# Optimization experiments

Measured on AMD Instinct MI355X. Metric: run time of the kernel, lower is better.

Reference implementation:

```python
import jax, jax.numpy as jnp
import numpy as np

N_NODES = 50000
N_EDGES = 800000
N_GRAPHS = 64
NEG_SLOPE = 0.2  # PyG GATConv default leaky_relu slope
EPS = 1e-16      # PyG softmax denominator epsilon


def gat_conv(x, W, a_src, a_dst, bias, src, dst, n_nodes):
    """PyG GATConv (heads=1, concat=True, self-loops already appended).
    x: [N, F_in], W: [F_in, H*F], a_src/a_dst: [H, F], bias: [H*F]."""
    H, F = a_src.shape
    h = (x @ W).reshape(-1, H, F)                      # [N, H, F]
    alpha_src = jnp.einsum('nhf,hf->nh', h, a_src)     # [N, H]
    alpha_dst = jnp.einsum('nhf,hf->nh', h, a_dst)     # [N, H]
    e = jax.nn.leaky_relu(alpha_src[src] + alpha_dst[dst], NEG_SLOPE)  # [E, H]
    # segment softmax over incoming edges of each destination node
    e_max = jax.ops.segment_max(e, dst, num_segments=n_nodes)          # [N, H]
    e_exp = jnp.exp(e - e_max[dst])
    denom = jax.ops.segment_sum(e_exp, dst, num_segments=n_nodes)      # [N, H]
    alpha = e_exp / (denom[dst] + EPS)                                 # [E, H]
    msg = alpha[:, :, None] * h[src]                                   # [E, H, F]
    out = jax.ops.segment_sum(msg, dst, num_segments=n_nodes)          # [N, H, F]
    return out.reshape(-1, H * F) + bias


def global_mean_pool(x, batch, n_graphs):
    s = jax.ops.segment_sum(x, batch, num_segments=n_graphs)
    cnt = jax.ops.segment_sum(jnp.ones((x.shape[0],), x.dtype), batch, num_segments=n_graphs)
    return s / jnp.maximum(cnt, 1.0)[:, None]


def setup_inputs() -> dict:
    key = jax.random.key(0)
    ks = jax.random.split(key, 10)
    d_in, d_h, d_out, L, H = 128, 128, 10, 3, 1
    x = jax.random.normal(ks[0], (N_NODES, d_in), dtype=jnp.float32)
    edge_index = jax.random.randint(ks[1], (2, N_EDGES), 0, N_NODES, dtype=jnp.int32)
    edge_attr = jax.random.normal(ks[2], (N_EDGES, 4), dtype=jnp.float32)
    batch = jnp.sort(jax.random.randint(ks[3], (N_NODES,), 0, N_GRAPHS, dtype=jnp.int32))
    s0 = 1.0 / np.sqrt(d_in)
    sh = 1.0 / np.sqrt(d_h)
    return {
        'x': x,
        'edge_index': edge_index,
        'edge_attr': edge_attr,
        'batch': batch,
        'W0': jax.random.normal(ks[4], (d_in, d_h), dtype=jnp.float32) * s0,
        'b0': jnp.zeros((d_h,), jnp.float32),
        'Wc': jax.random.normal(ks[5], (L, d_h, H * d_h), dtype=jnp.float32) * sh,
        'att_src': jax.random.normal(ks[6], (L, H, d_h), dtype=jnp.float32) * sh,
        'att_dst': jax.random.normal(ks[7], (L, H, d_h), dtype=jnp.float32) * sh,
        'bc': jnp.zeros((L, H * d_h), jnp.float32),
        'W1': jax.random.normal(ks[8], (d_h, d_out), dtype=jnp.float32) * sh,
        'b1': jnp.zeros((d_out,), jnp.float32),
    }


def reference(x, edge_index, edge_attr, batch, W0, b0, Wc, att_src, att_dst, bc, W1, b1):
    n = x.shape[0]
    # GATConv default add_self_loops=True
    loops = jnp.arange(n, dtype=edge_index.dtype)
    src = jnp.concatenate([edge_index[0], loops])
    dst = jnp.concatenate([edge_index[1], loops])
    # dropout p=0 / eval mode -> identity
    h = jax.nn.relu(x @ W0 + b0)
    for i in range(Wc.shape[0]):
        h = jax.nn.relu(gat_conv(h, Wc[i], att_src[i], att_dst[i], bc[i], src, dst, n))
    pooled = global_mean_pool(h, batch, N_GRAPHS)   # [B, d_h]
    return pooled @ W1 + b1                          # [B, d_out]
```

## Files before the change

kernel.cpp:

```cpp
#include <hip/hip_runtime.h>
#include <hip/hip_bf16.h>
#include <hip/hip_fp16.h>
#include <hip/hip_fp8.h>

#define NN 50000
#define NE 800000
#define NG 64
#define DH 128

#define SEG 64
#define GEMMB 512
#define GEMMW (GEMMB * 4)
#define CST 136
#define CSTB 136
#define SMEM_BYTES 17408
#define NPAIR (NN / 2)
#define NXCD 8
#define XNODES (NN / NXCD)
#define CHUNKE 4096
#define NCHUNK ((NE + CHUNKE - 1) / CHUNKE)
#define SCATB (NCHUNK * NXCD)
#define WTB 256
#define INITB ((NN + 255) / 256)
#define PREPB (SCATB + WTB + INITB)

#if defined(__has_builtin)
# if __has_builtin(__builtin_amdgcn_cvt_pk_f32_fp8) && __has_builtin(__builtin_amdgcn_cvt_pk_f32_fp8)
# endif
# if __has_builtin(__builtin_amdgcn_cvt_pk_f32_fp8) && __has_builtin(__builtin_amdgcn_cvt_pk_fp8_f32)
#  define HW_FP8 1
# endif
#endif

typedef __bf16 bfx8 __attribute__((ext_vector_type(8)));
typedef float  f32x4 __attribute__((ext_vector_type(4)));
typedef float  f32x8 __attribute__((ext_vector_type(8)));

__device__ __forceinline__ ushort f2b(float f) {
    unsigned b = __float_as_uint(f);
    b += 0x7fff + ((b >> 16) & 1);
    return (ushort)(b >> 16);
}
__device__ __forceinline__ float b2f(ushort s) {
    return __uint_as_float((unsigned)s << 16);
}
__device__ __forceinline__ unsigned pk2(float a, float b) {
    return (unsigned)f2b(a) | ((unsigned)f2b(b) << 16);
}

__device__ __forceinline__ unsigned f2fp8(float v) {
    v = fminf(fmaxf(v, -448.f), 448.f);
#ifdef HW_FP8
    return (unsigned)__builtin_amdgcn_cvt_pk_fp8_f32(v, v, 0, false) & 0xFFu;
#else
    __hip_fp8_e4m3 t(v);
    return (unsigned)*(const unsigned char*)&t;
#endif
}
__device__ __forceinline__ void fp8x4_up(unsigned u, float* o) {
#ifdef HW_FP8
    auto lo = __builtin_amdgcn_cvt_pk_f32_fp8((int)u, false);
    auto hi = __builtin_amdgcn_cvt_pk_f32_fp8((int)u, true);
    o[0] = lo[0]; o[1] = lo[1]; o[2] = hi[0]; o[3] = hi[1];
#else
    #pragma unroll
    for (int k = 0; k < 4; ++k) {
        unsigned char c = (u >> (8 * k)) & 0xFF;
        o[k] = float(*(const __hip_fp8_e4m3*)&c);
    }
#endif
}

__launch_bounds__(256)
__global__ void k_prep(const int* __restrict__ ei, int* __restrict__ cur,
                       ushort* __restrict__ csr,
                       const float* __restrict__ W0, const float* __restrict__ Wc,
                       ushort* __restrict__ Wt) {
    int t = threadIdx.x;
    unsigned bid = blockIdx.x;
    if (bid < SCATB) {
        int chunk = bid >> 3;
        int lo = (int)(bid & 7) * XNODES;
        int base = chunk * CHUNKE + t;
        #pragma unroll
        for (int jj = 0; jj < 16; jj += 4) {
            int dd[4], ee[4];
            #pragma unroll
            for (int q = 0; q < 4; ++q) {
                ee[q] = base + (jj + q) * 256;
                dd[q] = (ee[q] < NE) ? ei[NE + ee[q]] : -1;
            }
            #pragma unroll
            for (int q = 0; q < 4; ++q) {
                if ((unsigned)(dd[q] - lo) < (unsigned)XNODES) {
                    int s = ei[ee[q]];
                    int slot = atomicAdd(&cur[dd[q]], 1);
                    if (slot < SEG - 1)
                        csr[((size_t)dd[q] << 6) + 1 + slot] = (ushort)s;
                }
            }
        }
        return;
    }
    if (bid < SCATB + WTB) {
        int i = (bid - SCATB) * 256 + t;
        int m = i >> 14;
        int r = i & 16383;
        int k = r >> 7, n = r & 127;
        const float* src = (m == 0) ? W0 : (Wc + (size_t)(m - 1) * DH * DH);
        Wt[(size_t)m * DH * DH + n * DH + k] = f2b(src[r]);
        return;
    }
    int n = (bid - SCATB - WTB) * 256 + t;
    if (n < NN) csr[(size_t)n << 6] = (ushort)n;
}

template<bool AF32, bool DOTS, bool OUTFP8>
__device__ __forceinline__ void gemm_body(char* smem, int gblk,
        const void* __restrict__ Av, const ushort* __restrict__ Wt,
        const float* __restrict__ bias, void* __restrict__ C, int relu,
        const float* __restrict__ avs, const float* __restrict__ avd,
        float* __restrict__ asrc, float* __restrict__ adst) {
    const int NT = NN / 16;
    int tid = threadIdx.x;
    int lane = tid & 63;
    int mrow = lane & 15;
    int quad = lane >> 4;
    int wid = (gblk * 256 + tid) >> 6;

    bfx8 b[4][8];
    #pragma unroll
    for (int ks = 0; ks < 4; ++ks) {
        int k0 = ks * 32 + quad * 8;
        #pragma unroll
        for (int t = 0; t < 8; ++t)
            b[ks][t] = *(const bfx8*)(Wt + (size_t)(t * 16 + mrow) * DH + k0);
    }
    float av[8], dv[8];
    if (DOTS) {
        #pragma unroll
        for (int t = 0; t < 8; ++t) {
            av[t] = avs[t * 16 + mrow];
            dv[t] = avd[t * 16 + mrow];
        }
    }

    for (int tile = wid; tile < NT; tile += GEMMW) {
        int row0 = tile * 16;
        int arow = row0 + mrow;

        bfx8 a[4];
        if (AF32) {
            f32x8 af[4];
            #pragma unroll
            for (int ks = 0; ks < 4; ++ks)
                af[ks] = *(const f32x8*)((const float*)Av + (size_t)arow * DH + ks * 32 + quad * 8);
            #pragma unroll
            for (int ks = 0; ks < 4; ++ks) {
                union { ushort s[8]; bfx8 v; } u;
                #pragma unroll
                for (int j = 0; j < 8; ++j) u.s[j] = f2b(af[ks][j]);
                a[ks] = u.v;
            }
        } else {
            #pragma unroll
            for (int ks = 0; ks < 4; ++ks)
                a[ks] = *(const bfx8*)((const ushort*)Av + (size_t)arow * DH + ks * 32 + quad * 8);
        }

        f32x4 acc[8];
        #pragma unroll
        for (int t = 0; t < 8; ++t)
            #pragma unroll
            for (int r = 0; r < 4; ++r) acc[t][r] = 0.f;

        #pragma unroll
        for (int ks = 0; ks < 4; ++ks)
            #pragma unroll
            for (int t = 0; t < 8; ++t)
                acc[t] = __builtin_amdgcn_mfma_f32_16x16x32_bf16(a[ks], b[ks][t], acc[t], 0, 0, 0);

        if (OUTFP8) {
            uchar* my = (uchar*)smem + (tid >> 6) * 16 * CSTB;
            #pragma unroll
            for (int t = 0; t < 8; ++t) {
                int col = t * 16 + mrow;
                float bv = bias ? bias[col] : 0.f;
                #pragma unroll
                for (int r = 0; r < 4; ++r) {
                    float v = acc[t][r] + bv;
                    if (relu) v = fmaxf(v, 0.f);
                    my[(quad * 4 + r) * CSTB + col] = (uchar)f2fp8(v);
                }
            }
            #pragma unroll
            for (int i = 0; i < 4; ++i) {
                int idx = i * 64 + lane;
                int row = idx >> 4;
                int c8 = idx & 15;
                uint2 u = *(const uint2*)(my + row * CSTB + c8 * 8);
                *(uint2*)((uchar*)C + (size_t)(row0 + row) * DH + c8 * 8) = u;
            }
        } else {
            ushort* my = (ushort*)smem + (tid >> 6) * 16 * CST;
            #pragma unroll
            for (int t = 0; t < 8; ++t) {
                int col = t * 16 + mrow;
                float bv = bias ? bias[col] : 0.f;
                #pragma unroll
                for (int r = 0; r < 4; ++r) {
                    float v = acc[t][r] + bv;
                    if (relu) v = fmaxf(v, 0.f);
                    my[(quad * 4 + r) * CST + col] = f2b(v);
                }
            }
            #pragma unroll
            for (int i = 0; i < 4; ++i) {
                int idx = i * 64 + lane;
                int row = idx >> 4;
                int c16 = idx & 15;
                uint4 u = *(const uint4*)(my + row * CST + c16 * 8);
                *(uint4*)((ushort*)C + (size_t)(row0 + row) * DH + c16 * 8) = u;
            }
        }

        if (DOTS) {
            int orow = row0 + quad * 4;
            #pragma unroll
            for (int r = 0; r < 4; ++r) {
                float ps = 0.f, pd = 0.f;
                #pragma unroll
                for (int t = 0; t < 8; ++t) {
                    ps += acc[t][r] * av[t];
                    pd += acc[t][r] * dv[t];
                }
                #pragma unroll
                for (int off = 1; off < 16; off <<= 1) {
                    ps += __shfl_xor(ps, off);
                    pd += __shfl_xor(pd, off);
                }
                if (mrow == 0) {
                    asrc[orow + r] = ps;
                    adst[orow + r] = pd;
                }
            }
        }
    }
}

__launch_bounds__(256)
__global__ void k_gemm1(const float* __restrict__ x, const ushort* __restrict__ Wt,
                        const float* __restrict__ b0, ushort* __restrict__ hB) {
    __shared__ char smem[SMEM_BYTES];
    gemm_body<true, false, false>(smem, blockIdx.x, x, Wt, b0, hB, 1,
                                  nullptr, nullptr, nullptr, nullptr);
}

__launch_bounds__(256)
__global__ void k_gemmdots(const ushort* __restrict__ hB, const ushort* __restrict__ Wt,
                           uchar* __restrict__ hA,
                           const float* __restrict__ avs, const float* __restrict__ avd,
                           float* __restrict__ asrc, float* __restrict__ adst) {
    __shared__ char smem[SMEM_BYTES];
    gemm_body<false, true, true>(smem, blockIdx.x, hB, Wt, nullptr, hA, 0,
                                 avs, avd, asrc, adst);
}

__device__ __forceinline__ void aggr_one(int wid, int lane,
        const uchar* __restrict__ h8, const float* __restrict__ asrc,
        const float* __restrict__ adst, const int* __restrict__ cur,
        const ushort* __restrict__ csr,
        const float* __restrict__ bias, ushort* __restrict__ hout) {
    int start = wid << 6;
    int cnt = min(cur[wid] + 1, SEG);
    float ad = adst[wid];

    int s = csr[start + lane];
    float e = -1e30f;
    if (lane < cnt) {
        float t = asrc[s] + ad;
        e = fmaxf(t, 0.f) + 0.2f * fminf(t, 0.f);
    }
    float m = e;
    #pragma unroll
    for (int off = 32; off; off >>= 1) m = fmaxf(m, __shfl_xor(m, off));
    float w = (lane < cnt) ? __expf(e - m) : 0.f;
    float dsum = w;
    #pragma unroll
    for (int off = 32; off; off >>= 1) dsum += __shfl_xor(dsum, off);

    int g = lane >> 4, fidx = lane & 15;
    float acc[8];
    #pragma unroll
    for (int k = 0; k < 8; ++k) acc[k] = 0.f;

    int steps = (cnt + 3) >> 2;
    const uint2* hp = (const uint2*)h8;
    for (int j = 0; j < steps; ++j) {
        int e0 = j * 4 + g;
        float w0 = __shfl(w, e0);
        int   s0 = __shfl(s, e0);
        uint2 u0 = hp[(size_t)s0 * 16 + fidx];
        float v[8];
        fp8x4_up(u0.x, v); fp8x4_up(u0.y, v + 4);
        #pragma unroll
        for (int k = 0; k < 8; ++k) acc[k] += w0 * v[k];
    }
    #pragma unroll
    for (int k = 0; k < 8; ++k) {
        acc[k] += __shfl_xor(acc[k], 16);
        acc[k] += __shfl_xor(acc[k], 32);
    }
    if (g == 0) {
        float inv = 1.f / (dsum + 1e-16f);
        const float4* bp = (const float4*)bias;
        float4 b0 = bp[fidx * 2], b1 = bp[fidx * 2 + 1];
        uint4 o;
        o.x = pk2(fmaxf(acc[0] * inv + b0.x, 0.f), fmaxf(acc[1] * inv + b0.y, 0.f));
        o.y = pk2(fmaxf(acc[2] * inv + b0.z, 0.f), fmaxf(acc[3] * inv + b0.w, 0.f));
        o.z = pk2(fmaxf(acc[4] * inv + b1.x, 0.f), fmaxf(acc[5] * inv + b1.y, 0.f));
        o.w = pk2(fmaxf(acc[6] * inv + b1.z, 0.f), fmaxf(acc[7] * inv + b1.w, 0.f));
        ((uint4*)hout)[(size_t)wid * 16 + fidx] = o;
    }
}

__launch_bounds__(256)
__global__ void k_aggr(const uchar* __restrict__ h8, const float* __restrict__ asrc,
                       const float* __restrict__ adst, const int* __restrict__ cur,
                       const ushort* __restrict__ csr,
                       const float* __restrict__ bias, ushort* __restrict__ hout) {
    int pid = (blockIdx.x * blockDim.x + threadIdx.x) >> 6;
    int lane = threadIdx.x & 63;
    if (pid >= NPAIR) return;
    int half = lane >> 5, hl = lane & 31;
    int nd = pid * 2 + half;
    int start = nd << 6;

    int cnt = min(cur[nd] + 1, SEG);
    int cother = __shfl_xor(cnt, 32);
    if (max(cnt, cother) <= 32) {
        float ad = adst[nd];
        int s = csr[start + hl];
        float e = -1e30f;
        if (hl < cnt) {
            float t = asrc[s] + ad;
            e = fmaxf(t, 0.f) + 0.2f * fminf(t, 0.f);
        }
        float m = e;
        #pragma unroll
        for (int off = 16; off; off >>= 1) m = fmaxf(m, __shfl_xor(m, off));
        float w = (hl < cnt) ? __expf(e - m) : 0.f;
        float dsum = w;
        #pragma unroll
        for (int off = 16; off; off >>= 1) dsum += __shfl_xor(dsum, off);

        int g = hl >> 4, fidx = hl & 15;
        int lbase = half * 32;
        float acc[8];
        #pragma unroll
        for (int k = 0; k < 8; ++k) acc[k] = 0.f;

        int steps = (cnt + 1) >> 1;
        const uint2* hp = (const uint2*)h8;
        int j = 0;
        for (; j + 3 < steps; j += 4) {
            int   e0 = j * 2 + g,       e1 = e0 + 2, e2 = e0 + 4, e3 = e0 + 6;
            float w0 = __shfl(w, lbase + e0), w1 = __shfl(w, lbase + e1);
            float w2 = __shfl(w, lbase + e2), w3 = __shfl(w, lbase + e3);
            int   s0 = __shfl(s, lbase + e0), s1 = __shfl(s, lbase + e1);
            int   s2 = __shfl(s, lbase + e2), s3 = __shfl(s, lbase + e3);
            uint2 u0 = hp[(size_t)s0 * 16 + fidx];
            uint2 u1 = hp[(size_t)s1 * 16 + fidx];
            uint2 u2 = hp[(size_t)s2 * 16 + fidx];
            uint2 u3 = hp[(size_t)s3 * 16 + fidx];
            float v[8];
            fp8x4_up(u0.x, v); fp8x4_up(u0.y, v + 4);
            #pragma unroll
            for (int k = 0; k < 8; ++k) acc[k] += w0 * v[k];
            fp8x4_up(u1.x, v); fp8x4_up(u1.y, v + 4);
            #pragma unroll
            for (int k = 0; k < 8; ++k) acc[k] += w1 * v[k];
            fp8x4_up(u2.x, v); fp8x4_up(u2.y, v + 4);
            #pragma unroll
            for (int k = 0; k < 8; ++k) acc[k] += w2 * v[k];
            fp8x4_up(u3.x, v); fp8x4_up(u3.y, v + 4);
            #pragma unroll
            for (int k = 0; k < 8; ++k) acc[k] += w3 * v[k];
        }
        for (; j < steps; ++j) {
            int   e0 = j * 2 + g;
            float w0 = __shfl(w, lbase + e0);
            int   s0 = __shfl(s, lbase + e0);
            uint2 u0 = hp[(size_t)s0 * 16 + fidx];
            float v[8];
            fp8x4_up(u0.x, v); fp8x4_up(u0.y, v + 4);
            #pragma unroll
            for (int k = 0; k < 8; ++k) acc[k] += w0 * v[k];
        }
        #pragma unroll
        for (int k = 0; k < 8; ++k) acc[k] += __shfl_xor(acc[k], 16);
        if (g == 0) {
            float inv = 1.f / (dsum + 1e-16f);
            const float4* bp = (const float4*)bias;
            float4 b0 = bp[fidx * 2], b1 = bp[fidx * 2 + 1];
            uint4 o;
            o.x = pk2(fmaxf(acc[0] * inv + b0.x, 0.f), fmaxf(acc[1] * inv + b0.y, 0.f));
            o.y = pk2(fmaxf(acc[2] * inv + b0.z, 0.f), fmaxf(acc[3] * inv + b0.w, 0.f));
            o.z = pk2(fmaxf(acc[4] * inv + b1.x, 0.f), fmaxf(acc[5] * inv + b1.y, 0.f));
            o.w = pk2(fmaxf(acc[6] * inv + b1.z, 0.f), fmaxf(acc[7] * inv + b1.w, 0.f));
            ((uint4*)hout)[(size_t)nd * 16 + fidx] = o;
        }
        return;
    }

    aggr_one(pid * 2,     lane, h8, asrc, adst, cur, csr, bias, hout);
    aggr_one(pid * 2 + 1, lane, h8, asrc, adst, cur, csr, bias, hout);
}

__launch_bounds__(256)
__global__ void k_pool(const ushort* __restrict__ h, const int* __restrict__ batch,
                       float* __restrict__ gsum, int* __restrict__ gcnt) {
    int slot = threadIdx.x >> 7;
    int f = threadIdx.x & 127;
    int n0 = blockIdx.x * 64;
    int n1 = min(n0 + 64, NN);
    int first = n0 + slot;
    if (first >= n1) return;
    int g0 = batch[n0], g1 = batch[n1 - 1];
    if (g0 == g1) {
        float acc = 0.f;
        for (int nd = first; nd < n1; nd += 2)
            acc += b2f(h[(size_t)nd * DH + f]);
        atomicAdd(&gsum[g0 * DH + f], acc);
        if (f == 0 && slot == 0) atomicAdd(&gcnt[g0], n1 - n0);
        return;
    }
    float acc = 0.f; int run = 0;
    int gcur = batch[first];
    for (int nd = first; nd < n1; nd += 2) {
        int g = batch[nd];
        if (g != gcur) {
            atomicAdd(&gsum[gcur * DH + f], acc);
            if (f == 0) atomicAdd(&gcnt[gcur], run);
            acc = 0.f; run = 0; gcur = g;
        }
        acc += b2f(h[(size_t)nd * DH + f]);
        run += 1;
    }
    atomicAdd(&gsum[gcur * DH + f], acc);
    if (f == 0) atomicAdd(&gcnt[gcur], run);
}

__global__ void k_final(const float* __restrict__ gsum, const int* __restrict__ gcnt,
                        const float* __restrict__ W1, const float* __restrict__ b1,
                        float* __restrict__ out) {
    int t = threadIdx.x;
    if (t >= NG * 10) return;
    int g = t / 10, o = t % 10;
    float inv = 1.f / fmaxf((float)gcnt[g], 1.f);
    float acc = 0.f;
    for (int f = 0; f < DH; ++f) acc += gsum[g * DH + f] * W1[f * 10 + o];
    out[t] = acc * inv + b1[o];
}

extern "C" void kernel_launch(void* const* d_in, const int* in_sizes, int n_in,
                              void* d_out, int out_size, void* d_ws, size_t ws_size,
                              hipStream_t stream) {
    const float* x       = (const float*)d_in[0];
    const int*   ei      = (const int*)d_in[1];
    const int*   batch   = (const int*)d_in[3];
    const float* W0      = (const float*)d_in[4];
    const float* b0      = (const float*)d_in[5];
    const float* Wc      = (const float*)d_in[6];
    const float* att_src = (const float*)d_in[7];
    const float* att_dst = (const float*)d_in[8];
    const float* bc      = (const float*)d_in[9];
    const float* W1      = (const float*)d_in[10];
    const float* b1      = (const float*)d_in[11];
    float* out = (float*)d_out;

    char* ws = (char*)d_ws;
    size_t off = 0;
    auto alloc = [&](size_t bytes) {
        void* p = ws + off;
        off += (bytes + 255) & ~(size_t)255;
        return p;
    };
    uchar*    hA     = (uchar*)alloc((size_t)NN * DH);
    ushort*   hB     = (ushort*)alloc((size_t)NN * DH * 2);
    ushort*   Wt     = (ushort*)alloc((size_t)4 * DH * DH * 2);
    ushort*   csr    = (ushort*)alloc((size_t)NN * SEG * 2);
    int*      cur    = (int*)alloc((size_t)NN * 4);
    float*    asrc   = (float*)alloc(NN * 4);
    float*    adst   = (float*)alloc(NN * 4);
    float*    gsum   = (float*)alloc(NG * DH * 4);
    int*      gcnt   = (int*)alloc(NG * 4);

    hipMemsetAsync(csr, 0, (size_t)NN * SEG * 2 + (size_t)NN * 4, stream);
    hipMemsetAsync(gsum, 0, NG * DH * 4 + 256, stream);

    k_prep<<<PREPB, 256, 0, stream>>>(ei, cur, csr, W0, Wc, Wt);
    k_gemm1<<<GEMMB, 256, 0, stream>>>(x, Wt, b0, hB);

    for (int l = 0; l < 3; ++l) {
        k_gemmdots<<<GEMMB, 256, 0, stream>>>(hB, Wt + (size_t)(l + 1) * DH * DH, hA,
                                              att_src + l * DH, att_dst + l * DH,
                                              asrc, adst);
        k_aggr<<<(NPAIR + 3) / 4, 256, 0, stream>>>(hA, asrc, adst, cur, csr,
                                                    bc + l * DH, hB);
    }

    k_pool<<<(NN + 63) / 64, 256, 0, stream>>>(hB, batch, gsum, gcnt);
    k_final<<<1, NG * 10, 0, stream>>>(gsum, gcnt, W1, b1, out);
}
```

Baseline: 302.0 us.

## Fuse pooling and final linear into one per-graph kernel, shrink memsets

Replaces the atomic-based mean-pool kernel and the separate final linear kernel with a single kernel that launches one block per graph. Each block binary-searches the sorted batch array for its node range, sums rows with 16-byte vector loads, reduces through shared memory and applies W1. The large memset of the CSR buffer is dropped, and CSR reads are masked to valid lanes so stale entries are never used. This removes two memsets' worth of traffic, the atomics and one launch, but leaves only 64 blocks for the pooling read, which may limit parallelism.

```diff
diff --git a/kernel.cpp b/kernel.cpp
--- a/kernel.cpp
+++ b/kernel.cpp
@@ -25,8 +25,6 @@
 #define PREPB (SCATB + WTB + INITB)
 
 #if defined(__has_builtin)
-# if __has_builtin(__builtin_amdgcn_cvt_pk_f32_fp8) && __has_builtin(__builtin_amdgcn_cvt_pk_f32_fp8)
-# endif
 # if __has_builtin(__builtin_amdgcn_cvt_pk_f32_fp8) && __has_builtin(__builtin_amdgcn_cvt_pk_fp8_f32)
 #  define HW_FP8 1
 # endif
@@ -35,6 +33,7 @@
 typedef __bf16 bfx8 __attribute__((ext_vector_type(8)));
 typedef float  f32x4 __attribute__((ext_vector_type(4)));
 typedef float  f32x8 __attribute__((ext_vector_type(8)));
+typedef short  s16x8 __attribute__((ext_vector_type(8)));
 
 __device__ __forceinline__ ushort f2b(float f) {
     unsigned b = __float_as_uint(f);
@@ -275,7 +274,7 @@
     int cnt = min(cur[wid] + 1, SEG);
     float ad = adst[wid];
 
-    int s = csr[start + lane];
+    int s = (lane < cnt) ? (int)csr[start + lane] : 0;
     float e = -1e30f;
     if (lane < cnt) {
         float t = asrc[s] + ad;
@@ -340,7 +339,7 @@
     int cother = __shfl_xor(cnt, 32);
     if (max(cnt, cother) <= 32) {
         float ad = adst[nd];
-        int s = csr[start + hl];
+        int s = (hl < cnt) ? (int)csr[start + hl] : 0;
         float e = -1e30f;
         if (hl < cnt) {
             float t = asrc[s] + ad;
@@ -418,49 +417,48 @@
 }
 
 __launch_bounds__(256)
-__global__ void k_pool(const ushort* __restrict__ h, const int* __restrict__ batch,
-                       float* __restrict__ gsum, int* __restrict__ gcnt) {
-    int slot = threadIdx.x >> 7;
-    int f = threadIdx.x & 127;
-    int n0 = blockIdx.x * 64;
-    int n1 = min(n0 + 64, NN);
-    int first = n0 + slot;
-    if (first >= n1) return;
-    int g0 = batch[n0], g1 = batch[n1 - 1];
-    if (g0 == g1) {
-        float acc = 0.f;
-        for (int nd = first; nd < n1; nd += 2)
-            acc += b2f(h[(size_t)nd * DH + f]);
-        atomicAdd(&gsum[g0 * DH + f], acc);
-        if (f == 0 && slot == 0) atomicAdd(&gcnt[g0], n1 - n0);
-        return;
-    }
-    float acc = 0.f; int run = 0;
-    int gcur = batch[first];
-    for (int nd = first; nd < n1; nd += 2) {
-        int g = batch[nd];
-        if (g != gcur) {
-            atomicAdd(&gsum[gcur * DH + f], acc);
-            if (f == 0) atomicAdd(&gcnt[gcur], run);
-            acc = 0.f; run = 0; gcur = g;
-        }
-        acc += b2f(h[(size_t)nd * DH + f]);
-        run += 1;
-    }
-    atomicAdd(&gsum[gcur * DH + f], acc);
-    if (f == 0) atomicAdd(&gcnt[gcur], run);
-}
-
-__global__ void k_final(const float* __restrict__ gsum, const int* __restrict__ gcnt,
-                        const float* __restrict__ W1, const float* __restrict__ b1,
-                        float* __restrict__ out) {
+__global__ void k_tail(const ushort* __restrict__ h, const int* __restrict__ batch,
+                       const float* __restrict__ W1, const float* __restrict__ b1,
+                       float* __restrict__ out) {
+    __shared__ float sv[16][128];
+    int g = blockIdx.x;
     int t = threadIdx.x;
-    if (t >= NG * 10) return;
-    int g = t / 10, o = t % 10;
-    float inv = 1.f / fmaxf((float)gcnt[g], 1.f);
-    float acc = 0.f;
-    for (int f = 0; f < DH; ++f) acc += gsum[g * DH + f] * W1[f * 10 + o];
-    out[t] = acc * inv + b1[o];
+
+    int a = 0, b = NN;
+    while (a < b) { int m = (a + b) >> 1; if (batch[m] < g) a = m + 1; else b = m; }
+    int lo = a;
+    b = NN;
+    while (a < b) { int m = (a + b) >> 1; if (batch[m] < g + 1) a = m + 1; else b = m; }
+    int hi = a;
+
+    int slot = t >> 4;
+    int f8 = (t & 15) * 8;
+    float acc[8];
+    #pragma unroll
+    for (int j = 0; j < 8; ++j) acc[j] = 0.f;
+    for (int nd = lo + slot; nd < hi; nd += 16) {
+        s16x8 v = *(const s16x8*)(h + (size_t)nd * DH + f8);
+        #pragma unroll
+        for (int j = 0; j < 8; ++j) acc[j] += b2f((ushort)v[j]);
+    }
+    #pragma unroll
+    for (int j = 0; j < 8; ++j) sv[slot][f8 + j] = acc[j];
+    __syncthreads();
+
+    if (t < 128) {
+        float s = 0.f;
+        #pragma unroll
+        for (int k = 0; k < 16; ++k) s += sv[k][t];
+        sv[0][t] = s;
+    }
+    __syncthreads();
+
+    if (t < 10) {
+        float inv = 1.f / fmaxf((float)(hi - lo), 1.f);
+        float d = 0.f;
+        for (int f = 0; f < DH; ++f) d += sv[0][f] * W1[f * 10 + t];
+        out[g * 10 + t] = d * inv + b1[t];
+    }
 }
 
 extern "C" void kernel_launch(void* const* d_in, const int* in_sizes, int n_in,
@@ -493,11 +491,8 @@
     int*      cur    = (int*)alloc((size_t)NN * 4);
     float*    asrc   = (float*)alloc(NN * 4);
     float*    adst   = (float*)alloc(NN * 4);
-    float*    gsum   = (float*)alloc(NG * DH * 4);
-    int*      gcnt   = (int*)alloc(NG * 4);
-
-    hipMemsetAsync(csr, 0, (size_t)NN * SEG * 2 + (size_t)NN * 4, stream);
-    hipMemsetAsync(gsum, 0, NG * DH * 4 + 256, stream);
+
+    hipMemsetAsync(cur, 0, (size_t)NN * 4, stream);
 
     k_prep<<<PREPB, 256, 0, stream>>>(ei, cur, csr, W0, Wc, Wt);
     k_gemm1<<<GEMMB, 256, 0, stream>>>(x, Wt, b0, hB);
@@ -510,6 +505,5 @@
                                                     bc + l * DH, hB);
     }
 
-    k_pool<<<(NN + 63) / 64, 256, 0, stream>>>(hB, batch, gsum, gcnt);
-    k_final<<<1, NG * 10, 0, stream>>>(gsum, gcnt, W1, b1, out);
-}
+    k_tail<<<NG, 256, 0, stream>>>(hB, batch, W1, b1, out);
+}
```

After: 296.6 us (median of 3 runs). Within noise of the previous version (-1.8%).
